# Kernel tuning notes

Measured on AMD Instinct MI355X. Metric: run time of the kernel, lower is better.

Reference implementation:

```python
import jax, jax.numpy as jnp
import numpy as np

N = 100000   # nodes
E = 600000   # edges
D = 128      # in_dim == hidden
L = 3        # n_layers
B = 64       # graphs in batch


def setup_inputs() -> dict:
    key = jax.random.key(0)
    ks = jax.random.split(key, 7)
    x = jax.random.normal(ks[0], (N, D), dtype=jnp.float32)
    edge_index = jax.random.randint(ks[1], (2, E), 0, N, dtype=jnp.int32)
    batch_vec = jnp.sort(jax.random.randint(ks[2], (N,), 0, B, dtype=jnp.int32))
    scale = 1.0 / np.sqrt(D)
    Ws_self = jax.random.normal(ks[3], (L, D, D), dtype=jnp.float32) * scale
    bs_self = jax.random.normal(ks[4], (L, D), dtype=jnp.float32) * 0.01
    Ws_neigh = jax.random.normal(ks[5], (L, D, D), dtype=jnp.float32) * scale
    bs_neigh = jax.random.normal(ks[6], (L, D), dtype=jnp.float32) * 0.01
    return {"x": x, "edge_index": edge_index, "batch_vec": batch_vec,
            "Ws_self": Ws_self, "bs_self": bs_self,
            "Ws_neigh": Ws_neigh, "bs_neigh": bs_neigh}


def reference(x, edge_index, batch_vec, Ws_self, bs_self, Ws_neigh, bs_neigh):
    src, dst = edge_index[0], edge_index[1]
    # in-degree per node (clamped to 1), constant across layers
    deg = jax.ops.segment_sum(jnp.ones((E,), x.dtype), dst, num_segments=N)
    deg = jnp.maximum(deg, 1.0)[:, None]                     # [N, 1]
    for l in range(L):
        # gather neighbor features and scatter-mean onto dst nodes
        agg = jax.ops.segment_sum(x[src], dst, num_segments=N) / deg  # [N, D]
        h = x @ Ws_self[l] + bs_self[l] + agg @ Ws_neigh[l] + bs_neigh[l]
        x = jax.nn.relu(h)                                   # dropout: eval-mode identity
    # graph-level scatter_mean pooling
    pooled = jax.ops.segment_sum(x, batch_vec, num_segments=B)          # [B, D]
    cnt = jax.ops.segment_sum(jnp.ones((N,), x.dtype), batch_vec, num_segments=B)
    return pooled / jnp.maximum(cnt, 1.0)[:, None]
```

## Files before the change

### kernel.cpp

```cpp
#include <hip/hip_runtime.h>

#define N_NODES 100000
#define N_EDGES 600000
#define DIM     128
#define NGRAPHS 64
#define NPAD    100096
#define BCAP    32

typedef short  short8 __attribute__((ext_vector_type(8)));
typedef float  f32x4  __attribute__((ext_vector_type(4)));

__device__ __forceinline__ void atomAddF(float* p, float v) { unsafeAtomicAdd(p, v); }

__device__ __forceinline__ unsigned short f2bf(float f) {
    unsigned int u = __builtin_bit_cast(unsigned int, f);
    u += 0x7fffu + ((u >> 16) & 1u);
    return (unsigned short)(u >> 16);
}
__device__ __forceinline__ float bflo2f(unsigned int packed) {
    return __builtin_bit_cast(float, packed << 16);
}
__device__ __forceinline__ float bfhi2f(unsigned int packed) {
    return __builtin_bit_cast(float, packed & 0xffff0000u);
}

__global__ void cast_kernel(const float* __restrict__ x, unsigned short* __restrict__ xb,
                            int* __restrict__ cursor, int* __restrict__ cnt,
                            float* __restrict__ outz) {
    int t = blockIdx.x * blockDim.x + threadIdx.x;
    if (t < NPAD) cursor[t] = 0;
    if (t < NGRAPHS) cnt[t] = 0;
    if (t < NGRAPHS * DIM) outz[t] = 0.0f;
    size_t i8 = (size_t)t * 8;
    if (i8 >= (size_t)NPAD * DIM) return;
    uint4 o = make_uint4(0, 0, 0, 0);
    if (i8 < (size_t)N_NODES * DIM) {
        float4 v0 = *reinterpret_cast<const float4*>(x + i8);
        float4 v1 = *reinterpret_cast<const float4*>(x + i8 + 4);
        o.x = (unsigned)f2bf(v0.x) | ((unsigned)f2bf(v0.y) << 16);
        o.y = (unsigned)f2bf(v0.z) | ((unsigned)f2bf(v0.w) << 16);
        o.z = (unsigned)f2bf(v1.x) | ((unsigned)f2bf(v1.y) << 16);
        o.w = (unsigned)f2bf(v1.z) | ((unsigned)f2bf(v1.w) << 16);
    }
    *reinterpret_cast<uint4*>(xb + i8) = o;
}

__global__ void prep_kernel(const float* __restrict__ Ws, const float* __restrict__ Wn,
                            const float* __restrict__ bs, const float* __restrict__ bn,
                            unsigned short* __restrict__ Btg, float* __restrict__ biasg) {
    int t = blockIdx.x * blockDim.x + threadIdx.x;
    if (t >= 3 * 128 * 256) return;
    int layer = t >> 15;
    int rem   = t & 32767;
    int k     = rem >> 7;
    int col   = rem & 127;
    float w = (k < 128) ? Ws[layer * 16384 + k * 128 + col]
                        : Wn[layer * 16384 + (k - 128) * 128 + col];
    Btg[layer * 32768 + col * 256 + (k ^ ((col & 7) << 3))] = f2bf(w);
    if (t < 3 * 128) biasg[t] = bs[t] + bn[t];
}

__global__ void fillcnt_kernel(const int* __restrict__ src, const int* __restrict__ dst,
                               int* __restrict__ bucket, int* __restrict__ cursor,
                               const int* __restrict__ batch, int* __restrict__ cnt) {
    __shared__ int bins[NGRAPHS];
    if (threadIdx.x < NGRAPHS) bins[threadIdx.x] = 0;
    __syncthreads();
    int t = blockIdx.x * blockDim.x + threadIdx.x;
    if (t < N_EDGES) {
        int d = dst[t];
        int pos = atomicAdd(&cursor[d], 1);
        if (pos < BCAP) bucket[d * BCAP + pos] = src[t];
    }
    if (t < N_NODES) atomicAdd(&bins[batch[t]], 1);
    __syncthreads();
    if (threadIdx.x < NGRAPHS && bins[threadIdx.x] != 0)
        atomicAdd(&cnt[threadIdx.x], bins[threadIdx.x]);
}

__launch_bounds__(256)
__global__ void gather_kernel(const unsigned short* __restrict__ x,
                              const int* __restrict__ bucket,
                              const int* __restrict__ cursor,
                              unsigned short* __restrict__ agg) {
    const int l16  = threadIdx.x & 15;
    const int node = blockIdx.x * 16 + (threadIdx.x >> 4);
    const int k = min(cursor[node], BCAP);
    const int* __restrict__ bl = bucket + (size_t)node * BCAP;
    const size_t co = (size_t)l16 * 8;
    float acc[8];
#pragma unroll
    for (int i = 0; i < 8; ++i) acc[i] = 0.f;

    int j = 0;
    for (; j + 4 <= k; j += 4) {
        int4 s4 = *reinterpret_cast<const int4*>(bl + j);
        uint4 v0 = *reinterpret_cast<const uint4*>(x + (size_t)s4.x * DIM + co);
        uint4 v1 = *reinterpret_cast<const uint4*>(x + (size_t)s4.y * DIM + co);
        uint4 v2 = *reinterpret_cast<const uint4*>(x + (size_t)s4.z * DIM + co);
        uint4 v3 = *reinterpret_cast<const uint4*>(x + (size_t)s4.w * DIM + co);
        acc[0] += bflo2f(v0.x) + bflo2f(v1.x) + bflo2f(v2.x) + bflo2f(v3.x);
        acc[1] += bfhi2f(v0.x) + bfhi2f(v1.x) + bfhi2f(v2.x) + bfhi2f(v3.x);
        acc[2] += bflo2f(v0.y) + bflo2f(v1.y) + bflo2f(v2.y) + bflo2f(v3.y);
        acc[3] += bfhi2f(v0.y) + bfhi2f(v1.y) + bfhi2f(v2.y) + bfhi2f(v3.y);
        acc[4] += bflo2f(v0.z) + bflo2f(v1.z) + bflo2f(v2.z) + bflo2f(v3.z);
        acc[5] += bfhi2f(v0.z) + bfhi2f(v1.z) + bfhi2f(v2.z) + bfhi2f(v3.z);
        acc[6] += bflo2f(v0.w) + bflo2f(v1.w) + bflo2f(v2.w) + bflo2f(v3.w);
        acc[7] += bfhi2f(v0.w) + bfhi2f(v1.w) + bfhi2f(v2.w) + bfhi2f(v3.w);
    }
    for (; j < k; ++j) {
        int s = bl[j];
        uint4 v = *reinterpret_cast<const uint4*>(x + (size_t)s * DIM + co);
        acc[0] += bflo2f(v.x); acc[1] += bfhi2f(v.x);
        acc[2] += bflo2f(v.y); acc[3] += bfhi2f(v.y);
        acc[4] += bflo2f(v.z); acc[5] += bfhi2f(v.z);
        acc[6] += bflo2f(v.w); acc[7] += bfhi2f(v.w);
    }
    const float inv = (k > 0) ? 1.0f / (float)k : 0.0f;
    uint4 o;
    o.x = (unsigned)f2bf(acc[0] * inv) | ((unsigned)f2bf(acc[1] * inv) << 16);
    o.y = (unsigned)f2bf(acc[2] * inv) | ((unsigned)f2bf(acc[3] * inv) << 16);
    o.z = (unsigned)f2bf(acc[4] * inv) | ((unsigned)f2bf(acc[5] * inv) << 16);
    o.w = (unsigned)f2bf(acc[6] * inv) | ((unsigned)f2bf(acc[7] * inv) << 16);
    *reinterpret_cast<uint4*>(agg + (size_t)node * DIM + co) = o;
}

__launch_bounds__(512)
__global__ void gemm_kernel(const unsigned short* __restrict__ X,
                            unsigned short* AGG,
                            const unsigned short* __restrict__ Btg,
                            const float* __restrict__ biasg) {
    __shared__ unsigned short Blds[128 * 256];

    const int tid  = threadIdx.x;
#pragma unroll
    for (int i = 0; i < 8; ++i) {
        int idx8 = (i * 512 + tid) * 8;
        *reinterpret_cast<uint4*>(Blds + idx8) =
            *reinterpret_cast<const uint4*>(Btg + idx8);
    }
    __syncthreads();

    const int wave = tid >> 6;
    const int lane = tid & 63;
    const int l15  = lane & 15;
    const int lk   = lane >> 4;
    const int row_base = blockIdx.x * 256 + wave * 32;
    const int swz = (l15 & 7) << 3;

    f32x4 bias4[8];
#pragma unroll
    for (int c = 0; c < 8; ++c)
        bias4[c] = *reinterpret_cast<const f32x4*>(biasg + c * 16 + lk * 4);

    f32x4 acc[2][8];
#pragma unroll
    for (int r = 0; r < 2; ++r)
#pragma unroll
        for (int c = 0; c < 8; ++c) acc[r][c] = (f32x4)0.f;

#pragma unroll 2
    for (int s = 0; s < 8; ++s) {
        const unsigned short* __restrict__ base = (s < 4) ? X : AGG;
        const int kofs = (s & 3) * 32 + lk * 8;
        short8 a0 = *reinterpret_cast<const short8*>(base + (size_t)(row_base + l15) * DIM + kofs);
        short8 a1 = *reinterpret_cast<const short8*>(base + (size_t)(row_base + 16 + l15) * DIM + kofs);
        const int kidx = s * 32 + lk * 8;
#pragma unroll
        for (int c = 0; c < 8; ++c) {
            short8 b = *reinterpret_cast<const short8*>(Blds + (c * 16 + l15) * 256 + (kidx ^ swz));
            acc[0][c] = __builtin_amdgcn_mfma_f32_16x16x32_bf16(b, a0, acc[0][c], 0, 0, 0);
            acc[1][c] = __builtin_amdgcn_mfma_f32_16x16x32_bf16(b, a1, acc[1][c], 0, 0, 0);
        }
    }

#pragma unroll
    for (int r = 0; r < 2; ++r) {
        const size_t rowoff = (size_t)(row_base + r * 16 + l15) * DIM;
#pragma unroll
        for (int c = 0; c < 8; ++c) {
            float f0 = fmaxf(acc[r][c][0] + bias4[c][0], 0.f);
            float f1 = fmaxf(acc[r][c][1] + bias4[c][1], 0.f);
            float f2 = fmaxf(acc[r][c][2] + bias4[c][2], 0.f);
            float f3 = fmaxf(acc[r][c][3] + bias4[c][3], 0.f);
            uint2 o;
            o.x = (unsigned)f2bf(f0) | ((unsigned)f2bf(f1) << 16);
            o.y = (unsigned)f2bf(f2) | ((unsigned)f2bf(f3) << 16);
            *reinterpret_cast<uint2*>(AGG + rowoff + c * 16 + lk * 4) = o;
        }
    }
}

__global__ void pool_kernel(const unsigned short* __restrict__ x,
                            const int* __restrict__ batch,
                            float* __restrict__ out) {
    int q = threadIdx.x;
    int node0 = blockIdx.x * 32;
    float local = 0.0f;
    int prev = batch[node0];
    for (int nd = node0; nd < node0 + 32; ++nd) {
        int b = batch[nd];
        if (b != prev) {
            atomAddF(&out[prev * DIM + q], local);
            local = 0.0f;
            prev = b;
        }
        local += bflo2f((unsigned int)x[(size_t)nd * DIM + q]);
    }
    atomAddF(&out[prev * DIM + q], local);
}

__global__ void div_kernel(float* __restrict__ out, const int* __restrict__ cnt) {
    int t = blockIdx.x * blockDim.x + threadIdx.x;
    if (t < NGRAPHS * DIM) out[t] *= 1.0f / (float)max(cnt[t >> 7], 1);
}

extern "C" void kernel_launch(void* const* d_in, const int* in_sizes, int n_in,
                              void* d_out, int out_size, void* d_ws, size_t ws_size,
                              hipStream_t stream) {
    const float* x        = (const float*)d_in[0];
    const int*   ei       = (const int*)d_in[1];
    const int*   src      = ei;
    const int*   dst      = ei + N_EDGES;
    const int*   batch    = (const int*)d_in[2];
    const float* Ws_self  = (const float*)d_in[3];
    const float* bs_self  = (const float*)d_in[4];
    const float* Ws_neigh = (const float*)d_in[5];
    const float* bs_neigh = (const float*)d_in[6];
    float* out = (float*)d_out;

    const size_t NB = (size_t)NPAD * DIM;
    unsigned short* xb     = (unsigned short*)d_ws;
    unsigned short* b0     = xb + NB;
    unsigned short* b1     = b0 + NB;
    unsigned short* Btg    = b1 + NB;
    float*          biasg  = (float*)(Btg + 3 * 32768);
    int*            bucket = (int*)(biasg + 384);
    int*            cursor = bucket + (size_t)NPAD * BCAP;
    int*            cnt    = cursor + NPAD;

    cast_kernel<<<(int)((NB / 8 + 255) / 256), 256, 0, stream>>>(x, xb, cursor, cnt, out);
    prep_kernel<<<384, 256, 0, stream>>>(Ws_self, Ws_neigh, bs_self, bs_neigh, Btg, biasg);
    fillcnt_kernel<<<(N_EDGES + 255) / 256, 256, 0, stream>>>(src, dst, bucket, cursor, batch, cnt);

    const int ga_grid = NPAD / 16;
    const int gm_grid = NPAD / 256;

    gather_kernel<<<ga_grid, 256, 0, stream>>>(xb, bucket, cursor, b1);
    gemm_kernel<<<gm_grid, 512, 0, stream>>>(xb, b1, Btg, biasg);
    gather_kernel<<<ga_grid, 256, 0, stream>>>(b1, bucket, cursor, b0);
    gemm_kernel<<<gm_grid, 512, 0, stream>>>(b1, b0, Btg + 32768, biasg + 128);
    gather_kernel<<<ga_grid, 256, 0, stream>>>(b0, bucket, cursor, b1);
    gemm_kernel<<<gm_grid, 512, 0, stream>>>(b0, b1, Btg + 65536, biasg + 256);

    pool_kernel<<<N_NODES / 32, DIM, 0, stream>>>(b1, batch, out);
    div_kernel<<<(NGRAPHS * DIM + 255) / 256, 256, 0, stream>>>(out, cnt);
}
```

Before: 292.1 us.

## Fuse neighbor gather into per-layer GEMM kernel and merge setup kernels

Each layer's scatter-mean gather now runs inside the GEMM kernel. The aggregated rows go into a swizzled LDS tile instead of a global buffer, and the self-feature A fragments are prefetched into registers. The cast, weight-prep and bucket-fill kernels are merged into one launch, with counters zeroed by a memset. The final divide is folded into the pooling atomics. This removes the global write and read of the aggregate and several launches. The cost is that the fused kernel uses about 128KB of LDS with one 512-thread block per CU, which lowers occupancy for the latency-bound random gather.

```diff
diff --git a/kernel.cpp b/kernel.cpp
--- a/kernel.cpp
+++ b/kernel.cpp
@@ -7,6 +7,10 @@
 #define NPAD    100096
 #define BCAP    32
 
+#define CAST_BLOCKS 6256
+#define PREP_BLOCKS 384
+#define FILL_BLOCKS 2344
+
 typedef short  short8 __attribute__((ext_vector_type(8)));
 typedef float  f32x4  __attribute__((ext_vector_type(4)));
 
@@ -24,147 +28,156 @@
     return __builtin_bit_cast(float, packed & 0xffff0000u);
 }
 
-__global__ void cast_kernel(const float* __restrict__ x, unsigned short* __restrict__ xb,
-                            int* __restrict__ cursor, int* __restrict__ cnt,
-                            float* __restrict__ outz) {
-    int t = blockIdx.x * blockDim.x + threadIdx.x;
-    if (t < NPAD) cursor[t] = 0;
-    if (t < NGRAPHS) cnt[t] = 0;
-    if (t < NGRAPHS * DIM) outz[t] = 0.0f;
-    size_t i8 = (size_t)t * 8;
-    if (i8 >= (size_t)NPAD * DIM) return;
-    uint4 o = make_uint4(0, 0, 0, 0);
-    if (i8 < (size_t)N_NODES * DIM) {
-        float4 v0 = *reinterpret_cast<const float4*>(x + i8);
-        float4 v1 = *reinterpret_cast<const float4*>(x + i8 + 4);
-        o.x = (unsigned)f2bf(v0.x) | ((unsigned)f2bf(v0.y) << 16);
-        o.y = (unsigned)f2bf(v0.z) | ((unsigned)f2bf(v0.w) << 16);
-        o.z = (unsigned)f2bf(v1.x) | ((unsigned)f2bf(v1.y) << 16);
-        o.w = (unsigned)f2bf(v1.z) | ((unsigned)f2bf(v1.w) << 16);
-    }
-    *reinterpret_cast<uint4*>(xb + i8) = o;
-}
-
-__global__ void prep_kernel(const float* __restrict__ Ws, const float* __restrict__ Wn,
-                            const float* __restrict__ bs, const float* __restrict__ bn,
-                            unsigned short* __restrict__ Btg, float* __restrict__ biasg) {
-    int t = blockIdx.x * blockDim.x + threadIdx.x;
-    if (t >= 3 * 128 * 256) return;
-    int layer = t >> 15;
-    int rem   = t & 32767;
-    int k     = rem >> 7;
-    int col   = rem & 127;
-    float w = (k < 128) ? Ws[layer * 16384 + k * 128 + col]
-                        : Wn[layer * 16384 + (k - 128) * 128 + col];
-    Btg[layer * 32768 + col * 256 + (k ^ ((col & 7) << 3))] = f2bf(w);
-    if (t < 3 * 128) biasg[t] = bs[t] + bn[t];
-}
-
-__global__ void fillcnt_kernel(const int* __restrict__ src, const int* __restrict__ dst,
-                               int* __restrict__ bucket, int* __restrict__ cursor,
-                               const int* __restrict__ batch, int* __restrict__ cnt) {
-    __shared__ int bins[NGRAPHS];
-    if (threadIdx.x < NGRAPHS) bins[threadIdx.x] = 0;
-    __syncthreads();
-    int t = blockIdx.x * blockDim.x + threadIdx.x;
-    if (t < N_EDGES) {
-        int d = dst[t];
-        int pos = atomicAdd(&cursor[d], 1);
-        if (pos < BCAP) bucket[d * BCAP + pos] = src[t];
-    }
-    if (t < N_NODES) atomicAdd(&bins[batch[t]], 1);
-    __syncthreads();
-    if (threadIdx.x < NGRAPHS && bins[threadIdx.x] != 0)
-        atomicAdd(&cnt[threadIdx.x], bins[threadIdx.x]);
-}
-
-__launch_bounds__(256)
-__global__ void gather_kernel(const unsigned short* __restrict__ x,
-                              const int* __restrict__ bucket,
-                              const int* __restrict__ cursor,
-                              unsigned short* __restrict__ agg) {
-    const int l16  = threadIdx.x & 15;
-    const int node = blockIdx.x * 16 + (threadIdx.x >> 4);
-    const int k = min(cursor[node], BCAP);
-    const int* __restrict__ bl = bucket + (size_t)node * BCAP;
-    const size_t co = (size_t)l16 * 8;
-    float acc[8];
-#pragma unroll
-    for (int i = 0; i < 8; ++i) acc[i] = 0.f;
-
-    int j = 0;
-    for (; j + 4 <= k; j += 4) {
-        int4 s4 = *reinterpret_cast<const int4*>(bl + j);
-        uint4 v0 = *reinterpret_cast<const uint4*>(x + (size_t)s4.x * DIM + co);
-        uint4 v1 = *reinterpret_cast<const uint4*>(x + (size_t)s4.y * DIM + co);
-        uint4 v2 = *reinterpret_cast<const uint4*>(x + (size_t)s4.z * DIM + co);
-        uint4 v3 = *reinterpret_cast<const uint4*>(x + (size_t)s4.w * DIM + co);
-        acc[0] += bflo2f(v0.x) + bflo2f(v1.x) + bflo2f(v2.x) + bflo2f(v3.x);
-        acc[1] += bfhi2f(v0.x) + bfhi2f(v1.x) + bfhi2f(v2.x) + bfhi2f(v3.x);
-        acc[2] += bflo2f(v0.y) + bflo2f(v1.y) + bflo2f(v2.y) + bflo2f(v3.y);
-        acc[3] += bfhi2f(v0.y) + bfhi2f(v1.y) + bfhi2f(v2.y) + bfhi2f(v3.y);
-        acc[4] += bflo2f(v0.z) + bflo2f(v1.z) + bflo2f(v2.z) + bflo2f(v3.z);
-        acc[5] += bfhi2f(v0.z) + bfhi2f(v1.z) + bfhi2f(v2.z) + bfhi2f(v3.z);
-        acc[6] += bflo2f(v0.w) + bflo2f(v1.w) + bflo2f(v2.w) + bflo2f(v3.w);
-        acc[7] += bfhi2f(v0.w) + bfhi2f(v1.w) + bfhi2f(v2.w) + bfhi2f(v3.w);
-    }
-    for (; j < k; ++j) {
-        int s = bl[j];
-        uint4 v = *reinterpret_cast<const uint4*>(x + (size_t)s * DIM + co);
-        acc[0] += bflo2f(v.x); acc[1] += bfhi2f(v.x);
-        acc[2] += bflo2f(v.y); acc[3] += bfhi2f(v.y);
-        acc[4] += bflo2f(v.z); acc[5] += bfhi2f(v.z);
-        acc[6] += bflo2f(v.w); acc[7] += bfhi2f(v.w);
-    }
-    const float inv = (k > 0) ? 1.0f / (float)k : 0.0f;
-    uint4 o;
-    o.x = (unsigned)f2bf(acc[0] * inv) | ((unsigned)f2bf(acc[1] * inv) << 16);
-    o.y = (unsigned)f2bf(acc[2] * inv) | ((unsigned)f2bf(acc[3] * inv) << 16);
-    o.z = (unsigned)f2bf(acc[4] * inv) | ((unsigned)f2bf(acc[5] * inv) << 16);
-    o.w = (unsigned)f2bf(acc[6] * inv) | ((unsigned)f2bf(acc[7] * inv) << 16);
-    *reinterpret_cast<uint4*>(agg + (size_t)node * DIM + co) = o;
-}
-
-__launch_bounds__(512)
-__global__ void gemm_kernel(const unsigned short* __restrict__ X,
-                            unsigned short* AGG,
-                            const unsigned short* __restrict__ Btg,
-                            const float* __restrict__ biasg) {
+__global__ void prep_all_kernel(const float* __restrict__ x, unsigned short* __restrict__ xb,
+                                float* __restrict__ outz,
+                                const float* __restrict__ Ws, const float* __restrict__ Wn,
+                                const float* __restrict__ bs, const float* __restrict__ bn,
+                                unsigned short* __restrict__ Btg, float* __restrict__ biasg,
+                                const int* __restrict__ src, const int* __restrict__ dst,
+                                int* __restrict__ bucket, int* __restrict__ cursor,
+                                const int* __restrict__ batch, int* __restrict__ cnt) {
+    const int b = blockIdx.x;
+    if (b < CAST_BLOCKS) {
+        int t = b * 256 + threadIdx.x;
+        if (t < NGRAPHS * DIM) outz[t] = 0.0f;
+        size_t i8 = (size_t)t * 8;
+        uint4 o = make_uint4(0, 0, 0, 0);
+        if (i8 < (size_t)N_NODES * DIM) {
+            float4 v0 = *reinterpret_cast<const float4*>(x + i8);
+            float4 v1 = *reinterpret_cast<const float4*>(x + i8 + 4);
+            o.x = (unsigned)f2bf(v0.x) | ((unsigned)f2bf(v0.y) << 16);
+            o.y = (unsigned)f2bf(v0.z) | ((unsigned)f2bf(v0.w) << 16);
+            o.z = (unsigned)f2bf(v1.x) | ((unsigned)f2bf(v1.y) << 16);
+            o.w = (unsigned)f2bf(v1.z) | ((unsigned)f2bf(v1.w) << 16);
+        }
+        *reinterpret_cast<uint4*>(xb + i8) = o;
+    } else if (b < CAST_BLOCKS + PREP_BLOCKS) {
+        int t = (b - CAST_BLOCKS) * 256 + threadIdx.x;
+        int layer = t >> 15;
+        int rem   = t & 32767;
+        int k     = rem >> 7;
+        int col   = rem & 127;
+        float w = (k < 128) ? Ws[layer * 16384 + k * 128 + col]
+                            : Wn[layer * 16384 + (k - 128) * 128 + col];
+        Btg[layer * 32768 + col * 256 + (k ^ ((col & 7) << 3))] = f2bf(w);
+        if (t < 3 * 128) biasg[t] = bs[t] + bn[t];
+    } else {
+        __shared__ int bins[NGRAPHS];
+        if (threadIdx.x < NGRAPHS) bins[threadIdx.x] = 0;
+        __syncthreads();
+        int t = (b - CAST_BLOCKS - PREP_BLOCKS) * 256 + threadIdx.x;
+        if (t < N_EDGES) {
+            int d = dst[t];
+            int pos = atomicAdd(&cursor[d], 1);
+            if (pos < BCAP) bucket[d * BCAP + pos] = src[t];
+        }
+        if (t < N_NODES) atomicAdd(&bins[batch[t]], 1);
+        __syncthreads();
+        if (threadIdx.x < NGRAPHS && bins[threadIdx.x] != 0)
+            atomicAdd(&cnt[threadIdx.x], bins[threadIdx.x]);
+    }
+}
+
+__launch_bounds__(512, 1)
+__global__ void layer_kernel(const unsigned short* __restrict__ X,
+                             unsigned short* __restrict__ OUT,
+                             const int* __restrict__ bucket,
+                             const int* __restrict__ cursor,
+                             const unsigned short* __restrict__ Btg,
+                             const float* __restrict__ biasg) {
     __shared__ unsigned short Blds[128 * 256];
+    __shared__ unsigned short Alds[256 * 128];
 
     const int tid  = threadIdx.x;
+    const int wave = tid >> 6;
+    const int lane = tid & 63;
+    const int l15  = lane & 15;
+    const int lk   = lane >> 4;
+    const int row0 = blockIdx.x * 256;
+    const int row_base = row0 + wave * 32;
+    const int swz = (l15 & 7) << 3;
+
+    short8 apref[4][2];
+#pragma unroll
+    for (int s = 0; s < 4; ++s) {
+        const int kofs = s * 32 + lk * 8;
+        apref[s][0] = *reinterpret_cast<const short8*>(X + (size_t)(row_base + l15) * DIM + kofs);
+        apref[s][1] = *reinterpret_cast<const short8*>(X + (size_t)(row_base + 16 + l15) * DIM + kofs);
+    }
+
 #pragma unroll
     for (int i = 0; i < 8; ++i) {
         int idx8 = (i * 512 + tid) * 8;
         *reinterpret_cast<uint4*>(Blds + idx8) =
             *reinterpret_cast<const uint4*>(Btg + idx8);
     }
+
+    {
+        const int l16 = tid & 15;
+        const size_t co = (size_t)l16 * 8;
+#pragma unroll 1
+        for (int p = 0; p < 8; ++p) {
+            const int rel  = p * 32 + (tid >> 4);
+            const int node = row0 + rel;
+            const int k = min(cursor[node], BCAP);
+            const int* __restrict__ bl = bucket + (size_t)node * BCAP;
+            float acc[8];
+#pragma unroll
+            for (int i = 0; i < 8; ++i) acc[i] = 0.f;
+            int j = 0;
+            for (; j + 4 <= k; j += 4) {
+                int4 s4 = *reinterpret_cast<const int4*>(bl + j);
+                uint4 v0 = *reinterpret_cast<const uint4*>(X + (size_t)s4.x * DIM + co);
+                uint4 v1 = *reinterpret_cast<const uint4*>(X + (size_t)s4.y * DIM + co);
+                uint4 v2 = *reinterpret_cast<const uint4*>(X + (size_t)s4.z * DIM + co);
+                uint4 v3 = *reinterpret_cast<const uint4*>(X + (size_t)s4.w * DIM + co);
+                acc[0] += bflo2f(v0.x) + bflo2f(v1.x) + bflo2f(v2.x) + bflo2f(v3.x);
+                acc[1] += bfhi2f(v0.x) + bfhi2f(v1.x) + bfhi2f(v2.x) + bfhi2f(v3.x);
+                acc[2] += bflo2f(v0.y) + bflo2f(v1.y) + bflo2f(v2.y) + bflo2f(v3.y);
+                acc[3] += bfhi2f(v0.y) + bfhi2f(v1.y) + bfhi2f(v2.y) + bfhi2f(v3.y);
+                acc[4] += bflo2f(v0.z) + bflo2f(v1.z) + bflo2f(v2.z) + bflo2f(v3.z);
+                acc[5] += bfhi2f(v0.z) + bfhi2f(v1.z) + bfhi2f(v2.z) + bfhi2f(v3.z);
+                acc[6] += bflo2f(v0.w) + bflo2f(v1.w) + bflo2f(v2.w) + bflo2f(v3.w);
+                acc[7] += bfhi2f(v0.w) + bfhi2f(v1.w) + bfhi2f(v2.w) + bfhi2f(v3.w);
+            }
+            for (; j < k; ++j) {
+                int s = bl[j];
+                uint4 v = *reinterpret_cast<const uint4*>(X + (size_t)s * DIM + co);
+                acc[0] += bflo2f(v.x); acc[1] += bfhi2f(v.x);
+                acc[2] += bflo2f(v.y); acc[3] += bfhi2f(v.y);
+                acc[4] += bflo2f(v.z); acc[5] += bfhi2f(v.z);
+                acc[6] += bflo2f(v.w); acc[7] += bfhi2f(v.w);
+            }
+            const float inv = (k > 0) ? 1.0f / (float)k : 0.0f;
+            uint4 o;
+            o.x = (unsigned)f2bf(acc[0] * inv) | ((unsigned)f2bf(acc[1] * inv) << 16);
+            o.y = (unsigned)f2bf(acc[2] * inv) | ((unsigned)f2bf(acc[3] * inv) << 16);
+            o.z = (unsigned)f2bf(acc[4] * inv) | ((unsigned)f2bf(acc[5] * inv) << 16);
+            o.w = (unsigned)f2bf(acc[6] * inv) | ((unsigned)f2bf(acc[7] * inv) << 16);
+            *reinterpret_cast<uint4*>(Alds + rel * 128 + ((l16 * 8) ^ ((rel & 7) << 3))) = o;
+        }
+    }
     __syncthreads();
 
-    const int wave = tid >> 6;
-    const int lane = tid & 63;
-    const int l15  = lane & 15;
-    const int lk   = lane >> 4;
-    const int row_base = blockIdx.x * 256 + wave * 32;
-    const int swz = (l15 & 7) << 3;
-
-    f32x4 bias4[8];
-#pragma unroll
-    for (int c = 0; c < 8; ++c)
-        bias4[c] = *reinterpret_cast<const f32x4*>(biasg + c * 16 + lk * 4);
-
     f32x4 acc[2][8];
 #pragma unroll
     for (int r = 0; r < 2; ++r)
 #pragma unroll
         for (int c = 0; c < 8; ++c) acc[r][c] = (f32x4)0.f;
 
-#pragma unroll 2
+#pragma unroll
     for (int s = 0; s < 8; ++s) {
-        const unsigned short* __restrict__ base = (s < 4) ? X : AGG;
         const int kofs = (s & 3) * 32 + lk * 8;
-        short8 a0 = *reinterpret_cast<const short8*>(base + (size_t)(row_base + l15) * DIM + kofs);
-        short8 a1 = *reinterpret_cast<const short8*>(base + (size_t)(row_base + 16 + l15) * DIM + kofs);
+        short8 a0, a1;
+        if (s < 4) {
+            a0 = apref[s][0];
+            a1 = apref[s][1];
+        } else {
+            const int r0 = wave * 32 + l15;
+            const int r1 = r0 + 16;
+            a0 = *reinterpret_cast<const short8*>(Alds + r0 * 128 + (kofs ^ ((r0 & 7) << 3)));
+            a1 = *reinterpret_cast<const short8*>(Alds + r1 * 128 + (kofs ^ ((r1 & 7) << 3)));
+        }
         const int kidx = s * 32 + lk * 8;
 #pragma unroll
         for (int c = 0; c < 8; ++c) {
@@ -173,6 +186,11 @@
             acc[1][c] = __builtin_amdgcn_mfma_f32_16x16x32_bf16(b, a1, acc[1][c], 0, 0, 0);
         }
     }
+
+    f32x4 bias4[8];
+#pragma unroll
+    for (int c = 0; c < 8; ++c)
+        bias4[c] = *reinterpret_cast<const f32x4*>(biasg + c * 16 + lk * 4);
 
 #pragma unroll
     for (int r = 0; r < 2; ++r) {
@@ -186,13 +204,14 @@
             uint2 o;
             o.x = (unsigned)f2bf(f0) | ((unsigned)f2bf(f1) << 16);
             o.y = (unsigned)f2bf(f2) | ((unsigned)f2bf(f3) << 16);
-            *reinterpret_cast<uint2*>(AGG + rowoff + c * 16 + lk * 4) = o;
+            *reinterpret_cast<uint2*>(OUT + rowoff + c * 16 + lk * 4) = o;
         }
     }
 }
 
 __global__ void pool_kernel(const unsigned short* __restrict__ x,
                             const int* __restrict__ batch,
+                            const int* __restrict__ cnt,
                             float* __restrict__ out) {
     int q = threadIdx.x;
     int node0 = blockIdx.x * 32;
@@ -201,18 +220,13 @@
     for (int nd = node0; nd < node0 + 32; ++nd) {
         int b = batch[nd];
         if (b != prev) {
-            atomAddF(&out[prev * DIM + q], local);
+            atomAddF(&out[prev * DIM + q], local / (float)max(cnt[prev], 1));
             local = 0.0f;
             prev = b;
         }
         local += bflo2f((unsigned int)x[(size_t)nd * DIM + q]);
     }
-    atomAddF(&out[prev * DIM + q], local);
-}
-
-__global__ void div_kernel(float* __restrict__ out, const int* __restrict__ cnt) {
-    int t = blockIdx.x * blockDim.x + threadIdx.x;
-    if (t < NGRAPHS * DIM) out[t] *= 1.0f / (float)max(cnt[t >> 7], 1);
+    atomAddF(&out[prev * DIM + q], local / (float)max(cnt[prev], 1));
 }
 
 extern "C" void kernel_launch(void* const* d_in, const int* in_sizes, int n_in,
@@ -239,20 +253,17 @@
     int*            cursor = bucket + (size_t)NPAD * BCAP;
     int*            cnt    = cursor + NPAD;
 
-    cast_kernel<<<(int)((NB / 8 + 255) / 256), 256, 0, stream>>>(x, xb, cursor, cnt, out);
-    prep_kernel<<<384, 256, 0, stream>>>(Ws_self, Ws_neigh, bs_self, bs_neigh, Btg, biasg);
-    fillcnt_kernel<<<(N_EDGES + 255) / 256, 256, 0, stream>>>(src, dst, bucket, cursor, batch, cnt);
-
-    const int ga_grid = NPAD / 16;
+    hipMemsetAsync(cursor, 0, (NPAD + NGRAPHS) * sizeof(int), stream);
+
+    prep_all_kernel<<<CAST_BLOCKS + PREP_BLOCKS + FILL_BLOCKS, 256, 0, stream>>>(
+        x, xb, out, Ws_self, Ws_neigh, bs_self, bs_neigh, Btg, biasg,
+        src, dst, bucket, cursor, batch, cnt);
+
     const int gm_grid = NPAD / 256;
 
-    gather_kernel<<<ga_grid, 256, 0, stream>>>(xb, bucket, cursor, b1);
-    gemm_kernel<<<gm_grid, 512, 0, stream>>>(xb, b1, Btg, biasg);
-    gather_kernel<<<ga_grid, 256, 0, stream>>>(b1, bucket, cursor, b0);
-    gemm_kernel<<<gm_grid, 512, 0, stream>>>(b1, b0, Btg + 32768, biasg + 128);
-    gather_kernel<<<ga_grid, 256, 0, stream>>>(b0, bucket, cursor, b1);
-    gemm_kernel<<<gm_grid, 512, 0, stream>>>(b0, b1, Btg + 65536, biasg + 256);
-
-    pool_kernel<<<N_NODES / 32, DIM, 0, stream>>>(b1, batch, out);
-    div_kernel<<<(NGRAPHS * DIM + 255) / 256, 256, 0, stream>>>(out, cnt);
-}
+    layer_kernel<<<gm_grid, 512, 0, stream>>>(xb, b0, bucket, cursor, Btg, biasg);
+    layer_kernel<<<gm_grid, 512, 0, stream>>>(b0, b1, bucket, cursor, Btg + 32768, biasg + 128);
+    layer_kernel<<<gm_grid, 512, 0, stream>>>(b1, b0, bucket, cursor, Btg + 65536, biasg + 256);
+
+    pool_kernel<<<N_NODES / 32, DIM, 0, stream>>>(b0, batch, cnt, out);
+}
```

Measured after the change: 375.3 us. 28.5% more time.

## Merge setup kernels, prefetch first eight neighbors in gather, fold mean into pooling

Applied to the files above, without the earlier changes.

The cast, weight-prep and bucket-fill kernels become one launch that branches on block index, and the cursor and count arrays are zeroed with a memset. The gather kernel now always issues eight neighbor loads up front. Missing neighbors are redirected to a zero padding row, so the loads need no branches. The GEMM masks padding rows to zero so that row stays valid, and the pooling kernel divides by the graph count before its atomic add, which removes the separate divide kernel. This cuts launch overhead and exposes more memory parallelism in the gather, at the cost of extra wasted loads for low-degree nodes.

```diff
diff --git a/kernel.cpp b/kernel.cpp
--- a/kernel.cpp
+++ b/kernel.cpp
@@ -7,6 +7,10 @@
 #define NPAD    100096
 #define BCAP    32
 
+#define CAST_BLOCKS 6256
+#define PREP_BLOCKS 384
+#define FILL_BLOCKS 2344
+
 typedef short  short8 __attribute__((ext_vector_type(8)));
 typedef float  f32x4  __attribute__((ext_vector_type(4)));
 
@@ -24,58 +28,54 @@
     return __builtin_bit_cast(float, packed & 0xffff0000u);
 }
 
-__global__ void cast_kernel(const float* __restrict__ x, unsigned short* __restrict__ xb,
-                            int* __restrict__ cursor, int* __restrict__ cnt,
-                            float* __restrict__ outz) {
-    int t = blockIdx.x * blockDim.x + threadIdx.x;
-    if (t < NPAD) cursor[t] = 0;
-    if (t < NGRAPHS) cnt[t] = 0;
-    if (t < NGRAPHS * DIM) outz[t] = 0.0f;
-    size_t i8 = (size_t)t * 8;
-    if (i8 >= (size_t)NPAD * DIM) return;
-    uint4 o = make_uint4(0, 0, 0, 0);
-    if (i8 < (size_t)N_NODES * DIM) {
-        float4 v0 = *reinterpret_cast<const float4*>(x + i8);
-        float4 v1 = *reinterpret_cast<const float4*>(x + i8 + 4);
-        o.x = (unsigned)f2bf(v0.x) | ((unsigned)f2bf(v0.y) << 16);
-        o.y = (unsigned)f2bf(v0.z) | ((unsigned)f2bf(v0.w) << 16);
-        o.z = (unsigned)f2bf(v1.x) | ((unsigned)f2bf(v1.y) << 16);
-        o.w = (unsigned)f2bf(v1.z) | ((unsigned)f2bf(v1.w) << 16);
-    }
-    *reinterpret_cast<uint4*>(xb + i8) = o;
-}
-
-__global__ void prep_kernel(const float* __restrict__ Ws, const float* __restrict__ Wn,
-                            const float* __restrict__ bs, const float* __restrict__ bn,
-                            unsigned short* __restrict__ Btg, float* __restrict__ biasg) {
-    int t = blockIdx.x * blockDim.x + threadIdx.x;
-    if (t >= 3 * 128 * 256) return;
-    int layer = t >> 15;
-    int rem   = t & 32767;
-    int k     = rem >> 7;
-    int col   = rem & 127;
-    float w = (k < 128) ? Ws[layer * 16384 + k * 128 + col]
-                        : Wn[layer * 16384 + (k - 128) * 128 + col];
-    Btg[layer * 32768 + col * 256 + (k ^ ((col & 7) << 3))] = f2bf(w);
-    if (t < 3 * 128) biasg[t] = bs[t] + bn[t];
-}
-
-__global__ void fillcnt_kernel(const int* __restrict__ src, const int* __restrict__ dst,
-                               int* __restrict__ bucket, int* __restrict__ cursor,
-                               const int* __restrict__ batch, int* __restrict__ cnt) {
-    __shared__ int bins[NGRAPHS];
-    if (threadIdx.x < NGRAPHS) bins[threadIdx.x] = 0;
-    __syncthreads();
-    int t = blockIdx.x * blockDim.x + threadIdx.x;
-    if (t < N_EDGES) {
-        int d = dst[t];
-        int pos = atomicAdd(&cursor[d], 1);
-        if (pos < BCAP) bucket[d * BCAP + pos] = src[t];
-    }
-    if (t < N_NODES) atomicAdd(&bins[batch[t]], 1);
-    __syncthreads();
-    if (threadIdx.x < NGRAPHS && bins[threadIdx.x] != 0)
-        atomicAdd(&cnt[threadIdx.x], bins[threadIdx.x]);
+__global__ void prep_all_kernel(const float* __restrict__ x, unsigned short* __restrict__ xb,
+                                float* __restrict__ outz,
+                                const float* __restrict__ Ws, const float* __restrict__ Wn,
+                                const float* __restrict__ bs, const float* __restrict__ bn,
+                                unsigned short* __restrict__ Btg, float* __restrict__ biasg,
+                                const int* __restrict__ src, const int* __restrict__ dst,
+                                int* __restrict__ bucket, int* __restrict__ cursor,
+                                const int* __restrict__ batch, int* __restrict__ cnt) {
+    const int b = blockIdx.x;
+    if (b < CAST_BLOCKS) {
+        int t = b * 256 + threadIdx.x;
+        if (t < NGRAPHS * DIM) outz[t] = 0.0f;
+        size_t i8 = (size_t)t * 8;
+        uint4 o = make_uint4(0, 0, 0, 0);
+        if (i8 < (size_t)N_NODES * DIM) {
+            float4 v0 = *reinterpret_cast<const float4*>(x + i8);
+            float4 v1 = *reinterpret_cast<const float4*>(x + i8 + 4);
+            o.x = (unsigned)f2bf(v0.x) | ((unsigned)f2bf(v0.y) << 16);
+            o.y = (unsigned)f2bf(v0.z) | ((unsigned)f2bf(v0.w) << 16);
+            o.z = (unsigned)f2bf(v1.x) | ((unsigned)f2bf(v1.y) << 16);
+            o.w = (unsigned)f2bf(v1.z) | ((unsigned)f2bf(v1.w) << 16);
+        }
+        *reinterpret_cast<uint4*>(xb + i8) = o;
+    } else if (b < CAST_BLOCKS + PREP_BLOCKS) {
+        int t = (b - CAST_BLOCKS) * 256 + threadIdx.x;
+        int layer = t >> 15;
+        int rem   = t & 32767;
+        int k     = rem >> 7;
+        int col   = rem & 127;
+        float w = (k < 128) ? Ws[layer * 16384 + k * 128 + col]
+                            : Wn[layer * 16384 + (k - 128) * 128 + col];
+        Btg[layer * 32768 + col * 256 + (k ^ ((col & 7) << 3))] = f2bf(w);
+        if (t < 3 * 128) biasg[t] = bs[t] + bn[t];
+    } else {
+        __shared__ int bins[NGRAPHS];
+        if (threadIdx.x < NGRAPHS) bins[threadIdx.x] = 0;
+        __syncthreads();
+        int t = (b - CAST_BLOCKS - PREP_BLOCKS) * 256 + threadIdx.x;
+        if (t < N_EDGES) {
+            int d = dst[t];
+            int pos = atomicAdd(&cursor[d], 1);
+            if (pos < BCAP) bucket[d * BCAP + pos] = src[t];
+        }
+        if (t < N_NODES) atomicAdd(&bins[batch[t]], 1);
+        __syncthreads();
+        if (threadIdx.x < NGRAPHS && bins[threadIdx.x] != 0)
+            atomicAdd(&cnt[threadIdx.x], bins[threadIdx.x]);
+    }
 }
 
 __launch_bounds__(256)
@@ -92,30 +92,61 @@
 #pragma unroll
     for (int i = 0; i < 8; ++i) acc[i] = 0.f;
 
-    int j = 0;
-    for (; j + 4 <= k; j += 4) {
-        int4 s4 = *reinterpret_cast<const int4*>(bl + j);
-        uint4 v0 = *reinterpret_cast<const uint4*>(x + (size_t)s4.x * DIM + co);
-        uint4 v1 = *reinterpret_cast<const uint4*>(x + (size_t)s4.y * DIM + co);
-        uint4 v2 = *reinterpret_cast<const uint4*>(x + (size_t)s4.z * DIM + co);
-        uint4 v3 = *reinterpret_cast<const uint4*>(x + (size_t)s4.w * DIM + co);
-        acc[0] += bflo2f(v0.x) + bflo2f(v1.x) + bflo2f(v2.x) + bflo2f(v3.x);
-        acc[1] += bfhi2f(v0.x) + bfhi2f(v1.x) + bfhi2f(v2.x) + bfhi2f(v3.x);
-        acc[2] += bflo2f(v0.y) + bflo2f(v1.y) + bflo2f(v2.y) + bflo2f(v3.y);
-        acc[3] += bfhi2f(v0.y) + bfhi2f(v1.y) + bfhi2f(v2.y) + bfhi2f(v3.y);
-        acc[4] += bflo2f(v0.z) + bflo2f(v1.z) + bflo2f(v2.z) + bflo2f(v3.z);
-        acc[5] += bfhi2f(v0.z) + bfhi2f(v1.z) + bfhi2f(v2.z) + bfhi2f(v3.z);
-        acc[6] += bflo2f(v0.w) + bflo2f(v1.w) + bflo2f(v2.w) + bflo2f(v3.w);
-        acc[7] += bfhi2f(v0.w) + bfhi2f(v1.w) + bfhi2f(v2.w) + bfhi2f(v3.w);
-    }
-    for (; j < k; ++j) {
-        int s = bl[j];
-        uint4 v = *reinterpret_cast<const uint4*>(x + (size_t)s * DIM + co);
-        acc[0] += bflo2f(v.x); acc[1] += bfhi2f(v.x);
-        acc[2] += bflo2f(v.y); acc[3] += bfhi2f(v.y);
-        acc[4] += bflo2f(v.z); acc[5] += bfhi2f(v.z);
-        acc[6] += bflo2f(v.w); acc[7] += bfhi2f(v.w);
-    }
+    int4 q0 = *reinterpret_cast<const int4*>(bl);
+    int4 q1 = *reinterpret_cast<const int4*>(bl + 4);
+    int s0 = (k > 0) ? q0.x : N_NODES;
+    int s1 = (k > 1) ? q0.y : N_NODES;
+    int s2 = (k > 2) ? q0.z : N_NODES;
+    int s3 = (k > 3) ? q0.w : N_NODES;
+    int s4 = (k > 4) ? q1.x : N_NODES;
+    int s5 = (k > 5) ? q1.y : N_NODES;
+    int s6 = (k > 6) ? q1.z : N_NODES;
+    int s7 = (k > 7) ? q1.w : N_NODES;
+    uint4 v0 = *reinterpret_cast<const uint4*>(x + (size_t)s0 * DIM + co);
+    uint4 v1 = *reinterpret_cast<const uint4*>(x + (size_t)s1 * DIM + co);
+    uint4 v2 = *reinterpret_cast<const uint4*>(x + (size_t)s2 * DIM + co);
+    uint4 v3 = *reinterpret_cast<const uint4*>(x + (size_t)s3 * DIM + co);
+    uint4 v4 = *reinterpret_cast<const uint4*>(x + (size_t)s4 * DIM + co);
+    uint4 v5 = *reinterpret_cast<const uint4*>(x + (size_t)s5 * DIM + co);
+    uint4 v6 = *reinterpret_cast<const uint4*>(x + (size_t)s6 * DIM + co);
+    uint4 v7 = *reinterpret_cast<const uint4*>(x + (size_t)s7 * DIM + co);
+    acc[0] += bflo2f(v0.x) + bflo2f(v1.x) + bflo2f(v2.x) + bflo2f(v3.x)
+            + bflo2f(v4.x) + bflo2f(v5.x) + bflo2f(v6.x) + bflo2f(v7.x);
+    acc[1] += bfhi2f(v0.x) + bfhi2f(v1.x) + bfhi2f(v2.x) + bfhi2f(v3.x)
+            + bfhi2f(v4.x) + bfhi2f(v5.x) + bfhi2f(v6.x) + bfhi2f(v7.x);
+    acc[2] += bflo2f(v0.y) + bflo2f(v1.y) + bflo2f(v2.y) + bflo2f(v3.y)
+            + bflo2f(v4.y) + bflo2f(v5.y) + bflo2f(v6.y) + bflo2f(v7.y);
+    acc[3] += bfhi2f(v0.y) + bfhi2f(v1.y) + bfhi2f(v2.y) + bfhi2f(v3.y)
+            + bfhi2f(v4.y) + bfhi2f(v5.y) + bfhi2f(v6.y) + bfhi2f(v7.y);
+    acc[4] += bflo2f(v0.z) + bflo2f(v1.z) + bflo2f(v2.z) + bflo2f(v3.z)
+            + bflo2f(v4.z) + bflo2f(v5.z) + bflo2f(v6.z) + bflo2f(v7.z);
+    acc[5] += bfhi2f(v0.z) + bfhi2f(v1.z) + bfhi2f(v2.z) + bfhi2f(v3.z)
+            + bfhi2f(v4.z) + bfhi2f(v5.z) + bfhi2f(v6.z) + bfhi2f(v7.z);
+    acc[6] += bflo2f(v0.w) + bflo2f(v1.w) + bflo2f(v2.w) + bflo2f(v3.w)
+            + bflo2f(v4.w) + bflo2f(v5.w) + bflo2f(v6.w) + bflo2f(v7.w);
+    acc[7] += bfhi2f(v0.w) + bfhi2f(v1.w) + bfhi2f(v2.w) + bfhi2f(v3.w)
+            + bfhi2f(v4.w) + bfhi2f(v5.w) + bfhi2f(v6.w) + bfhi2f(v7.w);
+
+    for (int j = 8; j < k; j += 4) {
+        int4 s4v = *reinterpret_cast<const int4*>(bl + j);
+        int t0 = s4v.x;
+        int t1 = (j + 1 < k) ? s4v.y : N_NODES;
+        int t2 = (j + 2 < k) ? s4v.z : N_NODES;
+        int t3 = (j + 3 < k) ? s4v.w : N_NODES;
+        uint4 w0 = *reinterpret_cast<const uint4*>(x + (size_t)t0 * DIM + co);
+        uint4 w1 = *reinterpret_cast<const uint4*>(x + (size_t)t1 * DIM + co);
+        uint4 w2 = *reinterpret_cast<const uint4*>(x + (size_t)t2 * DIM + co);
+        uint4 w3 = *reinterpret_cast<const uint4*>(x + (size_t)t3 * DIM + co);
+        acc[0] += bflo2f(w0.x) + bflo2f(w1.x) + bflo2f(w2.x) + bflo2f(w3.x);
+        acc[1] += bfhi2f(w0.x) + bfhi2f(w1.x) + bfhi2f(w2.x) + bfhi2f(w3.x);
+        acc[2] += bflo2f(w0.y) + bflo2f(w1.y) + bflo2f(w2.y) + bflo2f(w3.y);
+        acc[3] += bfhi2f(w0.y) + bfhi2f(w1.y) + bfhi2f(w2.y) + bfhi2f(w3.y);
+        acc[4] += bflo2f(w0.z) + bflo2f(w1.z) + bflo2f(w2.z) + bflo2f(w3.z);
+        acc[5] += bfhi2f(w0.z) + bfhi2f(w1.z) + bfhi2f(w2.z) + bfhi2f(w3.z);
+        acc[6] += bflo2f(w0.w) + bflo2f(w1.w) + bflo2f(w2.w) + bflo2f(w3.w);
+        acc[7] += bfhi2f(w0.w) + bfhi2f(w1.w) + bfhi2f(w2.w) + bfhi2f(w3.w);
+    }
+
     const float inv = (k > 0) ? 1.0f / (float)k : 0.0f;
     uint4 o;
     o.x = (unsigned)f2bf(acc[0] * inv) | ((unsigned)f2bf(acc[1] * inv) << 16);
@@ -176,13 +207,15 @@
 
 #pragma unroll
     for (int r = 0; r < 2; ++r) {
-        const size_t rowoff = (size_t)(row_base + r * 16 + l15) * DIM;
+        const int row = row_base + r * 16 + l15;
+        const float mask = (row < N_NODES) ? 1.0f : 0.0f;
+        const size_t rowoff = (size_t)row * DIM;
 #pragma unroll
         for (int c = 0; c < 8; ++c) {
-            float f0 = fmaxf(acc[r][c][0] + bias4[c][0], 0.f);
-            float f1 = fmaxf(acc[r][c][1] + bias4[c][1], 0.f);
-            float f2 = fmaxf(acc[r][c][2] + bias4[c][2], 0.f);
-            float f3 = fmaxf(acc[r][c][3] + bias4[c][3], 0.f);
+            float f0 = fmaxf(acc[r][c][0] + bias4[c][0], 0.f) * mask;
+            float f1 = fmaxf(acc[r][c][1] + bias4[c][1], 0.f) * mask;
+            float f2 = fmaxf(acc[r][c][2] + bias4[c][2], 0.f) * mask;
+            float f3 = fmaxf(acc[r][c][3] + bias4[c][3], 0.f) * mask;
             uint2 o;
             o.x = (unsigned)f2bf(f0) | ((unsigned)f2bf(f1) << 16);
             o.y = (unsigned)f2bf(f2) | ((unsigned)f2bf(f3) << 16);
@@ -193,6 +226,7 @@
 
 __global__ void pool_kernel(const unsigned short* __restrict__ x,
                             const int* __restrict__ batch,
+                            const int* __restrict__ cnt,
                             float* __restrict__ out) {
     int q = threadIdx.x;
     int node0 = blockIdx.x * 32;
@@ -201,18 +235,13 @@
     for (int nd = node0; nd < node0 + 32; ++nd) {
         int b = batch[nd];
         if (b != prev) {
-            atomAddF(&out[prev * DIM + q], local);
+            atomAddF(&out[prev * DIM + q], local / (float)max(cnt[prev], 1));
             local = 0.0f;
             prev = b;
         }
         local += bflo2f((unsigned int)x[(size_t)nd * DIM + q]);
     }
-    atomAddF(&out[prev * DIM + q], local);
-}
-
-__global__ void div_kernel(float* __restrict__ out, const int* __restrict__ cnt) {
-    int t = blockIdx.x * blockDim.x + threadIdx.x;
-    if (t < NGRAPHS * DIM) out[t] *= 1.0f / (float)max(cnt[t >> 7], 1);
+    atomAddF(&out[prev * DIM + q], local / (float)max(cnt[prev], 1));
 }
 
 extern "C" void kernel_launch(void* const* d_in, const int* in_sizes, int n_in,
@@ -239,9 +268,11 @@
     int*            cursor = bucket + (size_t)NPAD * BCAP;
     int*            cnt    = cursor + NPAD;
 
-    cast_kernel<<<(int)((NB / 8 + 255) / 256), 256, 0, stream>>>(x, xb, cursor, cnt, out);
-    prep_kernel<<<384, 256, 0, stream>>>(Ws_self, Ws_neigh, bs_self, bs_neigh, Btg, biasg);
-    fillcnt_kernel<<<(N_EDGES + 255) / 256, 256, 0, stream>>>(src, dst, bucket, cursor, batch, cnt);
+    hipMemsetAsync(cursor, 0, (NPAD + NGRAPHS) * sizeof(int), stream);
+
+    prep_all_kernel<<<CAST_BLOCKS + PREP_BLOCKS + FILL_BLOCKS, 256, 0, stream>>>(
+        x, xb, out, Ws_self, Ws_neigh, bs_self, bs_neigh, Btg, biasg,
+        src, dst, bucket, cursor, batch, cnt);
 
     const int ga_grid = NPAD / 16;
     const int gm_grid = NPAD / 256;
@@ -253,6 +284,5 @@
     gather_kernel<<<ga_grid, 256, 0, stream>>>(b0, bucket, cursor, b1);
     gemm_kernel<<<gm_grid, 512, 0, stream>>>(b0, b1, Btg + 65536, biasg + 256);
 
-    pool_kernel<<<N_NODES / 32, DIM, 0, stream>>>(b1, batch, out);
-    div_kernel<<<(NGRAPHS * DIM + 255) / 256, 256, 0, stream>>>(out, cnt);
-}
+    pool_kernel<<<N_NODES / 32, DIM, 0, stream>>>(b1, batch, cnt, out);
+}
```

Measured after the change: 289.2 us. About the same (-1.0%).
